# Optimization experiments

Measured on AMD Instinct MI355X. Metric: run time of the kernel, lower is better.

## Reference

```python
import jax, jax.numpy as jnp
import numpy as np

HIDDEN = 1024
NUM_TOTAL = 8
NUM_SHARED = 2
NUM_ROUTED = NUM_TOTAL - NUM_SHARED
TOP_K = 2
TOKENS = 16384
SCALE = 0.02


def setup_inputs() -> dict:
    key = jax.random.key(0)
    ks = jax.random.split(key, 12)
    h = HIDDEN
    inp = {
        "x": jax.random.normal(ks[0], (TOKENS, h), dtype=jnp.float32),
        # shared experts: [E_s, in, hidden] / [E_s, hidden] etc. (y = x @ W + b)
        "shared_w1": jax.random.normal(ks[1], (NUM_SHARED, h, h), jnp.float32) * SCALE,
        "shared_b1": jnp.zeros((NUM_SHARED, h), jnp.float32),
        "shared_w2": jax.random.normal(ks[2], (NUM_SHARED, h, h), jnp.float32) * SCALE,
        "shared_b2": jnp.zeros((NUM_SHARED, h), jnp.float32),
        # routed experts
        "routed_w1": jax.random.normal(ks[3], (NUM_ROUTED, h, h), jnp.float32) * SCALE,
        "routed_b1": jnp.zeros((NUM_ROUTED, h), jnp.float32),
        "routed_w2": jax.random.normal(ks[4], (NUM_ROUTED, h, h), jnp.float32) * SCALE,
        "routed_b2": jnp.zeros((NUM_ROUTED, h), jnp.float32),
        # router: Linear(hidden, num_routed)
        "router_w": jax.random.normal(ks[5], (h, NUM_ROUTED), jnp.float32) * SCALE,
        "router_b": jnp.zeros((NUM_ROUTED,), jnp.float32),
    }
    return inp


def _expert_all(x, w1, b1, w2, b2):
    # x: [B, H]; w1/w2: [E, H, H]; returns [B, E, H]
    hmid = jnp.tanh(jnp.einsum("bi,eio->beo", x, w1) + b1)
    return jnp.einsum("beh,eho->beo", hmid, w2) + b2


def reference(x, shared_w1, shared_b1, shared_w2, shared_b2,
              routed_w1, routed_b1, routed_w2, routed_b2,
              router_w, router_b):
    # shared experts: every token through every shared expert, summed
    shared_out = _expert_all(x, shared_w1, shared_b1, shared_w2, shared_b2).sum(axis=1)  # [B,H]

    # router softmax + top-k mask (original weights each expert by
    # routing_weights[:, i] * mask[:, i], i.e. NOT renormalized)
    logits = x @ router_w + router_b                       # [B, E_r]
    routing_weights = jax.nn.softmax(logits, axis=-1)      # [B, E_r]
    _, top_idx = jax.lax.top_k(routing_weights, TOP_K)     # [B, k]
    mask = jax.nn.one_hot(top_idx, NUM_ROUTED, dtype=routing_weights.dtype).sum(axis=1)  # [B, E_r]
    weight = routing_weights * mask                        # [B, E_r]

    # dense all-expert compute masked by top-k (faithful to source loop)
    expert_out = _expert_all(x, routed_w1, routed_b1, routed_w2, routed_b2)  # [B, E_r, H]
    routed_out = jnp.einsum("be,beh->bh", weight, expert_out)

    return shared_out + routed_out
```

## Files before the change

### kernel.cpp

```cpp
#include <hip/hip_runtime.h>
#include <hip/hip_bf16.h>

#define H 1024
#define B_TOK 16384
#define RTILES 262
#define RCAP   (RTILES * 128)

typedef __attribute__((ext_vector_type(8))) short s16x8;
typedef __attribute__((ext_vector_type(4))) float f32x4;

__device__ __forceinline__ short f2bf(float f) {
  __hip_bfloat16 h = __float2bfloat16(f);
  return __builtin_bit_cast(short, h);
}
__device__ __forceinline__ float bf2f(short s) {
  __hip_bfloat16 h = __builtin_bit_cast(__hip_bfloat16, s);
  return __bfloat162float(h);
}

__device__ __forceinline__ void load_lds16(const short* g, short* l) {
  __builtin_amdgcn_global_load_lds((const __attribute__((address_space(1))) void*)g,
                                   (__attribute__((address_space(3))) void*)l,
                                   16, 0, 0);
}

__global__ void cvt_x_k(const float* __restrict__ x, short* __restrict__ xb) {
  const size_t i = ((size_t)blockIdx.x * blockDim.x + threadIdx.x) * 8;
  const float4 a = *(const float4*)(x + i);
  const float4 b = *(const float4*)(x + i + 4);
  s16x8 v;
  v[0] = f2bf(a.x); v[1] = f2bf(a.y); v[2] = f2bf(a.z); v[3] = f2bf(a.w);
  v[4] = f2bf(b.x); v[5] = f2bf(b.y); v[6] = f2bf(b.z); v[7] = f2bf(b.w);
  *(s16x8*)(xb + i) = v;
}

__global__ void transpose_k(const float* __restrict__ sw1, const float* __restrict__ rw1,
                            const float* __restrict__ sw2, const float* __restrict__ rw2,
                            short* __restrict__ w1t, short* __restrict__ w2t_sh,
                            short* __restrict__ w2t_r) {
  __shared__ float tile[64][65];
  const int z = blockIdx.z;
  const float* src;
  short* dst;
  int ldd = H, koff = 0;
  if (z < 8) {
    src = (z < 2) ? sw1 + (size_t)z * H * H : rw1 + (size_t)(z - 2) * H * H;
    dst = w1t + (size_t)z * H * H;
  } else if (z < 10) {
    const int e = z - 8;
    src = sw2 + (size_t)e * H * H;
    dst = w2t_sh; ldd = 2048; koff = e * 1024;
  } else {
    const int e = z - 10;
    src = rw2 + (size_t)e * H * H;
    dst = w2t_r + (size_t)e * H * H;
  }
  const int k0 = blockIdx.y * 64, n0 = blockIdx.x * 64;
  const int t = threadIdx.x;
#pragma unroll
  for (int i = 0; i < 4; ++i) {
    const int kk = (t >> 4) + 16 * i;
    const int nn = (t & 15) * 4;
    const float4 v = *(const float4*)(src + (size_t)(k0 + kk) * H + n0 + nn);
    tile[nn + 0][kk] = v.x; tile[nn + 1][kk] = v.y;
    tile[nn + 2][kk] = v.z; tile[nn + 3][kk] = v.w;
  }
  __syncthreads();
  const int nn = t >> 2;
  const int kk = (t & 3) * 16;
  s16x8 o0, o1;
#pragma unroll
  for (int u = 0; u < 8; ++u) {
    o0[u] = f2bf(tile[nn][kk + u]);
    o1[u] = f2bf(tile[nn][kk + 8 + u]);
  }
  short* drow = dst + (size_t)(n0 + nn) * ldd + koff + k0 + kk;
  *(s16x8*)(drow) = o0;
  *(s16x8*)(drow + 8) = o1;
}

__global__ void logits_k(const float* __restrict__ x, const float* __restrict__ rw,
                         const float* __restrict__ rb, int2* __restrict__ tk) {
  const int lane = threadIdx.x & 63;
  const int b = blockIdx.x * 4 + (threadIdx.x >> 6);
  const float* xr = x + (size_t)b * H;
  float p[6] = {0.f, 0.f, 0.f, 0.f, 0.f, 0.f};
  for (int k = lane; k < H; k += 64) {
    const float xv = xr[k];
    const float* r = rw + k * 6;
#pragma unroll
    for (int e = 0; e < 6; ++e) p[e] += xv * r[e];
  }
#pragma unroll
  for (int e = 0; e < 6; ++e) {
    float v = p[e];
    for (int off = 32; off > 0; off >>= 1) v += __shfl_down(v, off);
    p[e] = v;
  }
  if (lane == 0) {
    float lg[6];
    float mx = -1e30f;
#pragma unroll
    for (int e = 0; e < 6; ++e) { lg[e] = p[e] + rb[e]; mx = fmaxf(mx, lg[e]); }
    float s = 0.f;
#pragma unroll
    for (int e = 0; e < 6; ++e) { lg[e] = __expf(lg[e] - mx); s += lg[e]; }
    const float inv = 1.f / s;
#pragma unroll
    for (int e = 0; e < 6; ++e) lg[e] *= inv;
    int i1 = 0;
#pragma unroll
    for (int e = 1; e < 6; ++e) if (lg[e] > lg[i1]) i1 = e;
    int i2 = (i1 == 0) ? 1 : 0;
#pragma unroll
    for (int e = 0; e < 6; ++e) if (e != i1 && lg[e] > lg[i2]) i2 = e;
    int2 v;
    v.x = i1 | ((int)(unsigned short)f2bf(lg[i1]) << 16);
    v.y = i2 | ((int)(unsigned short)f2bf(lg[i2]) << 16);
    tk[b] = v;
  }
}

__global__ void hist_k(const int2* __restrict__ tk, int* __restrict__ g) {
  __shared__ int h[6];
  const int t = threadIdx.x;
  if (t < 6) h[t] = 0;
  __syncthreads();
  const int2 v = tk[blockIdx.x * 256 + t];
  atomicAdd(&h[v.x & 0xffff], 1);
  atomicAdd(&h[v.y & 0xffff], 1);
  __syncthreads();
  if (t < 6) atomicAdd(&g[t], h[t]);
}

__global__ void prefix_k(int* __restrict__ g) {
  if (threadIdx.x == 0) {
    int run = 0;
#pragma unroll
    for (int e = 0; e < 6; ++e) {
      g[8 + e] = run; g[16 + e] = run;
      run += (g[e] + 127) & ~127;
    }
    g[14] = run;
  }
}

__global__ void scatter_k(const int2* __restrict__ tk, int* __restrict__ g,
                          int* __restrict__ asg) {
  __shared__ int lcnt[6];
  __shared__ int lbase[6];
  const int t = threadIdx.x;
  if (t < 6) lcnt[t] = 0;
  __syncthreads();
  const int tok = blockIdx.x * 256 + t;
  const int2 v = tk[tok];
  const int e1 = v.x & 0xffff, e2 = v.y & 0xffff;
  const int p1 = atomicAdd(&lcnt[e1], 1);
  const int p2 = atomicAdd(&lcnt[e2], 1);
  __syncthreads();
  if (t < 6) lbase[t] = atomicAdd(&g[16 + t], lcnt[t]);
  __syncthreads();
  asg[lbase[e1] + p1] = tok | (v.x & 0xffff0000);
  asg[lbase[e2] + p2] = tok | (v.y & 0xffff0000);
}

__device__ __forceinline__ void gemm_core64(const short* __restrict__ A, int lda,
                                            const short* __restrict__ Bt, int ldb, int K,
                                            short* smem, int m0, int n0,
                                            const int* __restrict__ asg, int acap,
                                            f32x4 acc[4][4]) {
  const int tid = threadIdx.x, lane = tid & 63, w = tid >> 6;
  const int q8 = (lane >> 4) * 8, r16 = lane & 15;
  const int wr = w >> 1, wc = w & 1;

  const short* gp[4];
#pragma unroll
  for (int ii = 0; ii < 4; ++ii) {
    const int c2 = w * 4 + ii;
    if (c2 < 8) {
      int slot = m0 + c2 * 16 + r16;
      int gr;
      if (asg) {
        int tv = asg[slot] & 0xffff;
        gr = tv < B_TOK ? tv : B_TOK - 1;
      } else {
        gr = slot < acap ? slot : acap - 1;
      }
      gp[ii] = A + (size_t)gr * lda + q8;
    } else {
      gp[ii] = Bt + (size_t)(n0 + (c2 - 8) * 16 + r16) * ldb + q8;
    }
  }
  short* lbase = smem + w * 4096;

  for (int k0 = 0; k0 < K; k0 += 64) {
    __syncthreads();
#pragma unroll
    for (int i = 0; i < 8; ++i)
      load_lds16(gp[i >> 1] + k0 + (i & 1) * 32, lbase + i * 512);
    __syncthreads();
#pragma unroll
    for (int s = 0; s < 2; ++s) {
      s16x8 af[4], bfv[4];
#pragma unroll
      for (int i = 0; i < 4; ++i)
        af[i] = *(const s16x8*)(smem + ((wr * 4 + i) * 2 + s) * 512 + lane * 8);
#pragma unroll
      for (int j = 0; j < 4; ++j)
        bfv[j] = *(const s16x8*)(smem + (16 + (wc * 4 + j) * 2 + s) * 512 + lane * 8);
#pragma unroll
      for (int i = 0; i < 4; ++i)
#pragma unroll
        for (int j = 0; j < 4; ++j)
          acc[i][j] = __builtin_amdgcn_mfma_f32_16x16x32_bf16(af[i], bfv[j], acc[i][j], 0, 0, 0);
    }
  }
}

template <int ROUTED>
__global__ __launch_bounds__(256) void gemm1_k(const short* __restrict__ A, int lda,
                                               const short* __restrict__ W1, int ldb, int K,
                                               const float* __restrict__ b1,
                                               short* __restrict__ Out, int ldo,
                                               const int* __restrict__ asg,
                                               const int* __restrict__ g, int rowcap) {
  const int m0 = blockIdx.x * 128, n0 = blockIdx.y * 128;
  const short* Bt = W1;
  const float* bias = b1;
  if (ROUTED) {
    if (m0 >= g[14]) return;
    int e = 0;
#pragma unroll
    for (int j = 1; j < 6; ++j) if (m0 >= g[8 + j]) e = j;
    Bt = W1 + (size_t)e * H * H;
    bias = b1 + (size_t)e * H;
  }
  __shared__ __align__(16) short smem[16384];
  f32x4 acc[4][4];
#pragma unroll
  for (int i = 0; i < 4; ++i)
#pragma unroll
    for (int j = 0; j < 4; ++j) acc[i][j] = (f32x4){0.f, 0.f, 0.f, 0.f};
  gemm_core64(A, lda, Bt, ldb, K, smem, m0, n0, ROUTED ? asg : nullptr, 1 << 30, acc);

  const int tid = threadIdx.x, lane = tid & 63, w = tid >> 6;
  const int wr = w >> 1, wc = w & 1, q = lane >> 4, c16 = lane & 15;
  __syncthreads();
#pragma unroll
  for (int j = 0; j < 4; ++j) {
    const int colL = wc * 64 + j * 16 + c16;
    const float bv = bias[n0 + colL];
#pragma unroll
    for (int i = 0; i < 4; ++i)
#pragma unroll
      for (int r = 0; r < 4; ++r)
        smem[(wr * 64 + i * 16 + q * 4 + r) * 128 + colL] = f2bf(tanhf(acc[i][j][r] + bv));
  }
  __syncthreads();
#pragma unroll
  for (int p = 0; p < 8; ++p) {
    const int rowL = p * 16 + (tid >> 4);
    const int colL = (tid & 15) * 8;
    const int gr = m0 + rowL;
    if (gr < rowcap)
      *(s16x8*)(Out + (size_t)gr * ldo + n0 + colL) = *(const s16x8*)(smem + rowL * 128 + colL);
  }
}

template <int MODE>
__global__ __launch_bounds__(256) void gemm2_k(const short* __restrict__ A, int lda,
                                               const short* __restrict__ W2, int ldb, int K,
                                               const float* __restrict__ b2a,
                                               const float* __restrict__ b2b,
                                               float* __restrict__ Out,
                                               const int* __restrict__ asg,
                                               const int* __restrict__ g, int acap) {
  const int m0 = blockIdx.x * 128, n0 = blockIdx.y * 128;
  const short* Bt = W2;
  const float* bias = b2a;
  if (MODE == 3) {
    if (m0 >= g[14]) return;
    int e = 0;
#pragma unroll
    for (int j = 1; j < 6; ++j) if (m0 >= g[8 + j]) e = j;
    Bt = W2 + (size_t)e * H * H;
    bias = b2a + (size_t)e * H;
  }
  __shared__ __align__(16) short smem[16384];
  f32x4 acc[4][4];
#pragma unroll
  for (int i = 0; i < 4; ++i)
#pragma unroll
    for (int j = 0; j < 4; ++j) acc[i][j] = (f32x4){0.f, 0.f, 0.f, 0.f};
  gemm_core64(A, lda, Bt, ldb, K, smem, m0, n0, nullptr, acap, acc);

  const int tid = threadIdx.x, lane = tid & 63, w = tid >> 6;
  const int wr = w >> 1, wc = w & 1, q = lane >> 4, c16 = lane & 15;

  if (MODE == 0) {
    float* cs = (float*)smem;
    __syncthreads();
#pragma unroll
    for (int half = 0; half < 2; ++half) {
      if (wr == half) {
#pragma unroll
        for (int j = 0; j < 4; ++j) {
          const int colL = wc * 64 + j * 16 + c16;
          const float bv = b2a[n0 + colL] + b2b[n0 + colL];
#pragma unroll
          for (int i = 0; i < 4; ++i)
#pragma unroll
            for (int r = 0; r < 4; ++r)
              cs[(i * 16 + q * 4 + r) * 128 + colL] = acc[i][j][r] + bv;
        }
      }
      __syncthreads();
#pragma unroll
      for (int p = 0; p < 8; ++p) {
        const int rowL = p * 8 + (tid >> 5);
        const int colL = (tid & 31) * 4;
        *(float4*)(Out + (size_t)(m0 + half * 64 + rowL) * H + n0 + colL) =
            *(const float4*)(cs + rowL * 128 + colL);
      }
      __syncthreads();
    }
  } else {
    const int mb = m0 + wr * 64, nb = n0 + wc * 64;
#pragma unroll
    for (int i = 0; i < 4; ++i) {
      int av[4];
#pragma unroll
      for (int r = 0; r < 4; ++r) av[r] = asg[mb + i * 16 + q * 4 + r];
#pragma unroll
      for (int j = 0; j < 4; ++j) {
        const int col = nb + j * 16 + c16;
        const float bv = bias[col];
#pragma unroll
        for (int r = 0; r < 4; ++r) {
          if (av[r] == -1) continue;
          const int tok = av[r] & 0xffff;
          const float wt = bf2f((short)((unsigned)av[r] >> 16));
          atomicAdd(&Out[(size_t)tok * H + col], (acc[i][j][r] + bv) * wt);
        }
      }
    }
  }
}

extern "C" void kernel_launch(void* const* d_in, const int* in_sizes, int n_in,
                              void* d_out, int out_size, void* d_ws, size_t ws_size,
                              hipStream_t stream) {
  const float* x        = (const float*)d_in[0];
  const float* sw1      = (const float*)d_in[1];
  const float* sb1      = (const float*)d_in[2];
  const float* sw2      = (const float*)d_in[3];
  const float* sb2      = (const float*)d_in[4];
  const float* rw1      = (const float*)d_in[5];
  const float* rb1      = (const float*)d_in[6];
  const float* rw2      = (const float*)d_in[7];
  const float* rb2      = (const float*)d_in[8];
  const float* router_w = (const float*)d_in[9];
  const float* router_b = (const float*)d_in[10];
  float* out = (float*)d_out;

  char* ws = (char*)d_ws;
  short* xb     = (short*)(ws);
  short* w1t    = (short*)(ws + (size_t)33554432);
  short* w2t_r  = (short*)(ws + (size_t)50331648);
  short* w2t_sh = (short*)(ws + (size_t)62914560);
  short* hm_sh  = (short*)(ws + (size_t)67108864);
  short* hm_r   = (short*)(ws + (size_t)62914560);
  int2*  tk     = (int2*)hm_sh;
  int*   g      = (int*)(ws + (size_t)134217728);
  int*   asg    = (int*)(ws + (size_t)134217984);

  hipMemsetAsync(g, 0, 64, stream);
  hipMemsetAsync(asg, 0xFF, RCAP * sizeof(int), stream);

  cvt_x_k<<<8192, 256, 0, stream>>>(x, xb);
  transpose_k<<<dim3(16, 16, 16), 256, 0, stream>>>(sw1, rw1, sw2, rw2, w1t, w2t_sh, w2t_r);
  logits_k<<<4096, 256, 0, stream>>>(x, router_w, router_b, tk);
  hist_k<<<64, 256, 0, stream>>>(tk, g);
  prefix_k<<<1, 64, 0, stream>>>(g);
  scatter_k<<<64, 256, 0, stream>>>(tk, g, asg);

  gemm1_k<0><<<dim3(128, 16), 256, 0, stream>>>(xb, H, w1t, H, H, sb1, hm_sh, 2048,
                                                nullptr, nullptr, 1 << 30);
  gemm2_k<0><<<dim3(128, 8), 256, 0, stream>>>(hm_sh, 2048, w2t_sh, 2048, 2048,
                                               sb2, sb2 + H, out, nullptr, nullptr, 1 << 30);

  gemm1_k<1><<<dim3(RTILES, 8), 256, 0, stream>>>(xb, H, w1t + (size_t)2 * H * H, H, H,
                                                  rb1, hm_r, H, asg, g, RCAP);
  gemm2_k<3><<<dim3(RTILES, 8), 256, 0, stream>>>(hm_r, H, w2t_r, H, H,
                                                  rb2, nullptr, out, asg, g, RCAP);
}
```

Before: 834.1 us.

## Split routed assignments by rank to replace output atomics with plain adds

Routed assignments are partitioned by top-k rank (first choice vs second choice) into separate per-expert segments, so each token appears at most once per segment. The second GEMM runs as two sequential launches, one per rank, and each can use a non-atomic read-modify-write on the output instead of atomicAdd. This removes atomic contention and atomic throughput costs in the epilogue. In exchange it adds an extra launch and more padded tiles, and the first launch uses a fixed grid of 134 tiles that could be too small if the rank-0 segment grows past it.

```diff
diff --git a/kernel.cpp b/kernel.cpp
--- a/kernel.cpp
+++ b/kernel.cpp
@@ -3,7 +3,7 @@
 
 #define H 1024
 #define B_TOK 16384
-#define RTILES 262
+#define RTILES 268
 #define RCAP   (RTILES * 128)
 
 typedef __attribute__((ext_vector_type(8))) short s16x8;
@@ -122,24 +122,25 @@
 }
 
 __global__ void hist_k(const int2* __restrict__ tk, int* __restrict__ g) {
-  __shared__ int h[6];
+  __shared__ int h[12];
   const int t = threadIdx.x;
-  if (t < 6) h[t] = 0;
+  if (t < 12) h[t] = 0;
   __syncthreads();
   const int2 v = tk[blockIdx.x * 256 + t];
   atomicAdd(&h[v.x & 0xffff], 1);
-  atomicAdd(&h[v.y & 0xffff], 1);
-  __syncthreads();
-  if (t < 6) atomicAdd(&g[t], h[t]);
+  atomicAdd(&h[6 + (v.y & 0xffff)], 1);
+  __syncthreads();
+  if (t < 12) atomicAdd(&g[t], h[t]);
 }
 
 __global__ void prefix_k(int* __restrict__ g) {
   if (threadIdx.x == 0) {
     int run = 0;
 #pragma unroll
-    for (int e = 0; e < 6; ++e) {
-      g[8 + e] = run; g[16 + e] = run;
-      run += (g[e] + 127) & ~127;
+    for (int r = 0; r < 12; ++r) {
+      g[32 + r] = run; g[48 + r] = run;
+      run += (g[r] + 127) & ~127;
+      if (r == 5) g[15] = run;
     }
     g[14] = run;
   }
@@ -147,21 +148,22 @@
 
 __global__ void scatter_k(const int2* __restrict__ tk, int* __restrict__ g,
                           int* __restrict__ asg) {
-  __shared__ int lcnt[6];
-  __shared__ int lbase[6];
+  __shared__ int lcnt[12];
+  __shared__ int lbase[12];
   const int t = threadIdx.x;
-  if (t < 6) lcnt[t] = 0;
+  if (t < 12) lcnt[t] = 0;
   __syncthreads();
   const int tok = blockIdx.x * 256 + t;
   const int2 v = tk[tok];
-  const int e1 = v.x & 0xffff, e2 = v.y & 0xffff;
-  const int p1 = atomicAdd(&lcnt[e1], 1);
-  const int p2 = atomicAdd(&lcnt[e2], 1);
-  __syncthreads();
-  if (t < 6) lbase[t] = atomicAdd(&g[16 + t], lcnt[t]);
-  __syncthreads();
-  asg[lbase[e1] + p1] = tok | (v.x & 0xffff0000);
-  asg[lbase[e2] + p2] = tok | (v.y & 0xffff0000);
+  const int r1 = v.x & 0xffff;
+  const int r2 = 6 + (v.y & 0xffff);
+  const int p1 = atomicAdd(&lcnt[r1], 1);
+  const int p2 = atomicAdd(&lcnt[r2], 1);
+  __syncthreads();
+  if (t < 12) lbase[t] = atomicAdd(&g[48 + t], lcnt[t]);
+  __syncthreads();
+  asg[lbase[r1] + p1] = tok | (v.x & 0xffff0000);
+  asg[lbase[r2] + p2] = tok | (v.y & 0xffff0000);
 }
 
 __device__ __forceinline__ void gemm_core64(const short* __restrict__ A, int lda,
@@ -229,9 +231,10 @@
   const float* bias = b1;
   if (ROUTED) {
     if (m0 >= g[14]) return;
-    int e = 0;
-#pragma unroll
-    for (int j = 1; j < 6; ++j) if (m0 >= g[8 + j]) e = j;
+    int r = 0;
+#pragma unroll
+    for (int j = 1; j < 12; ++j) if (m0 >= g[32 + j]) r = j;
+    const int e = r % 6;
     Bt = W1 + (size_t)e * H * H;
     bias = b1 + (size_t)e * H;
   }
@@ -274,15 +277,19 @@
                                                const float* __restrict__ b2b,
                                                float* __restrict__ Out,
                                                const int* __restrict__ asg,
-                                               const int* __restrict__ g, int acap) {
+                                               const int* __restrict__ g, int acap,
+                                               int rank) {
   const int m0 = blockIdx.x * 128, n0 = blockIdx.y * 128;
   const short* Bt = W2;
   const float* bias = b2a;
   if (MODE == 3) {
-    if (m0 >= g[14]) return;
-    int e = 0;
-#pragma unroll
-    for (int j = 1; j < 6; ++j) if (m0 >= g[8 + j]) e = j;
+    const int lo = rank ? g[15] : 0;
+    const int hi = rank ? g[14] : g[15];
+    if (m0 < lo || m0 >= hi) return;
+    int r = 0;
+#pragma unroll
+    for (int j = 1; j < 12; ++j) if (m0 >= g[32 + j]) r = j;
+    const int e = r % 6;
     Bt = W2 + (size_t)e * H * H;
     bias = b2a + (size_t)e * H;
   }
@@ -340,7 +347,8 @@
           if (av[r] == -1) continue;
           const int tok = av[r] & 0xffff;
           const float wt = bf2f((short)((unsigned)av[r] >> 16));
-          atomicAdd(&Out[(size_t)tok * H + col], (acc[i][j][r] + bv) * wt);
+          float* p = &Out[(size_t)tok * H + col];
+          *p += (acc[i][j][r] + bv) * wt;
         }
       }
     }
@@ -387,10 +395,13 @@
   gemm1_k<0><<<dim3(128, 16), 256, 0, stream>>>(xb, H, w1t, H, H, sb1, hm_sh, 2048,
                                                 nullptr, nullptr, 1 << 30);
   gemm2_k<0><<<dim3(128, 8), 256, 0, stream>>>(hm_sh, 2048, w2t_sh, 2048, 2048,
-                                               sb2, sb2 + H, out, nullptr, nullptr, 1 << 30);
+                                               sb2, sb2 + H, out, nullptr, nullptr,
+                                               1 << 30, 0);
 
   gemm1_k<1><<<dim3(RTILES, 8), 256, 0, stream>>>(xb, H, w1t + (size_t)2 * H * H, H, H,
                                                   rb1, hm_r, H, asg, g, RCAP);
+  gemm2_k<3><<<dim3(134, 8), 256, 0, stream>>>(hm_r, H, w2t_r, H, H,
+                                               rb2, nullptr, out, asg, g, RCAP, 0);
   gemm2_k<3><<<dim3(RTILES, 8), 256, 0, stream>>>(hm_r, H, w2t_r, H, H,
-                                                  rb2, nullptr, out, asg, g, RCAP);
-}
+                                                  rb2, nullptr, out, asg, g, RCAP, 1);
+}
```

Result: slower. 905.2 us (+8.5%).
